# Kernel tuning notes

Hardware: AMD Instinct MI355X
Metric: run time of the kernel (lower is better)

The kernel has to match this reference:

```python
import jax, jax.numpy as jnp
import numpy as np

B, S, H, D = 8, 1024, 16, 64
W = H * D  # hidden width = 1024


def setup_inputs() -> dict:
    key = jax.random.key(0)
    ks = jax.random.split(key, 5)
    std = 0.02
    return {
        "from_tensor": jax.random.normal(ks[0], (B, S, W), dtype=jnp.float32),
        "to_tensor": jax.random.normal(ks[1], (B, S, W), dtype=jnp.float32),
        "Wq": jax.random.normal(ks[2], (W, W), dtype=jnp.float32) * std,
        "bq": jnp.zeros((W,), dtype=jnp.float32),
        "Wk": jax.random.normal(ks[3], (W, W), dtype=jnp.float32) * std,
        "bk": jnp.zeros((W,), dtype=jnp.float32),
        "Wv": jax.random.normal(ks[4], (W, W), dtype=jnp.float32) * std,
        "bv": jnp.zeros((W,), dtype=jnp.float32),
    }


def reference(from_tensor, to_tensor, Wq, bq, Wk, bk, Wv, bv):
    # Q/K/V projections (no activations: query_act=key_act=value_act=None)
    q = from_tensor @ Wq + bq  # [B, S, W]
    k = to_tensor @ Wk + bk
    v = to_tensor @ Wv + bv
    # split heads -> [B, H, S, D]
    q = q.reshape(B, S, H, D).transpose(0, 2, 1, 3)
    k = k.reshape(B, S, H, D).transpose(0, 2, 1, 3)
    v = v.reshape(B, S, H, D).transpose(0, 2, 1, 3)
    scale = 1.0 / np.sqrt(float(D))
    scores = jnp.einsum("bhqd,bhkd->bhqk", q, k) * scale  # [B, H, S, S]
    # attention_mask=None, dropout_prob=0.0 -> no mask, no dropout
    probs = jax.nn.softmax(scores, axis=-1)
    ctx = jnp.einsum("bhqk,bhkd->bhqd", probs, v)  # [B, H, S, D]
    # merge heads -> [B, S, H*D] (do_return_2d_tensor=False)
    return ctx.transpose(0, 2, 1, 3).reshape(B, S, H * D)
```

## Files before the change

### kernel.cpp

```cpp
#include <hip/hip_runtime.h>
#include <hip/hip_bf16.h>
#include <math.h>


#define B_ 8
#define S_ 1024
#define H_ 16
#define D_ 64
#define W_ 1024

typedef __bf16 bf16x8 __attribute__((ext_vector_type(8)));
typedef float f32x4 __attribute__((ext_vector_type(4)));
typedef unsigned short ushort_t;

#define MFMA16(a, b, c) __builtin_amdgcn_mfma_f32_16x16x32_bf16((a), (b), (c), 0, 0, 0)

__device__ inline ushort_t f2bf(float f) {
    unsigned int u = __float_as_uint(f);
    u += 0x7fff + ((u >> 16) & 1);
    return (ushort_t)(u >> 16);
}

__device__ inline unsigned f2bf_rhu_u(float f) {
    return (__float_as_uint(f) + 0x8000u) >> 16;
}

__device__ inline void async16(const void* g, void* l) {
    __builtin_amdgcn_global_load_lds((const __attribute__((address_space(1))) void*)g,
                                     (__attribute__((address_space(3))) void*)l, 16, 0, 0);
}

__global__ __launch_bounds__(256) void cast2_bf16(const float* __restrict__ a,
                                                  const float* __restrict__ b,
                                                  ushort_t* __restrict__ da,
                                                  ushort_t* __restrict__ db, int n4) {
    int i = blockIdx.x * 256 + threadIdx.x;
    if (i >= n4) return;
    const float* src = blockIdx.y ? b : a;
    ushort_t* dst = blockIdx.y ? db : da;
    float4 v = ((const float4*)src)[i];
    ushort4 o;
    o.x = f2bf(v.x); o.y = f2bf(v.y); o.z = f2bf(v.z); o.w = f2bf(v.w);
    ((ushort4*)dst)[i] = o;
}

__global__ __launch_bounds__(256) void transpose_cast(const float* __restrict__ Wq,
                                                      const float* __restrict__ Wk,
                                                      const float* __restrict__ Wv,
                                                      ushort_t* __restrict__ Wt) {
    __shared__ float tile[32][33];
    int z = blockIdx.z;
    const float* src = (z == 0) ? Wq : (z == 1 ? Wk : Wv);
    ushort_t* dst = Wt + (size_t)z * W_ * W_;
    int tx = threadIdx.x, ty = threadIdx.y;
    int x = blockIdx.x * 32 + tx;
#pragma unroll
    for (int jj = 0; jj < 4; jj++) {
        int y = blockIdx.y * 32 + ty + jj * 8;
        tile[ty + jj * 8][tx] = src[(size_t)y * W_ + x];
    }
    __syncthreads();
    int x2 = blockIdx.y * 32 + tx;
#pragma unroll
    for (int jj = 0; jj < 4; jj++) {
        int y2 = blockIdx.x * 32 + ty + jj * 8;
        dst[(size_t)y2 * W_ + x2] = f2bf(tile[tx][ty + jj * 8]);
    }
}

__global__ __launch_bounds__(256) void qkv_gemm(const ushort_t* __restrict__ fromB,
                                                const ushort_t* __restrict__ toB,
                                                const ushort_t* __restrict__ Wt,
                                                const float* __restrict__ bq,
                                                const float* __restrict__ bk,
                                                const float* __restrict__ bv,
                                                ushort_t* __restrict__ Qd,
                                                ushort_t* __restrict__ Kd,
                                                ushort_t* __restrict__ Vt) {
    __shared__ __attribute__((aligned(16))) ushort_t As[128 * 32];
    __shared__ __attribute__((aligned(16))) ushort_t Bs[128 * 32];
    int z = blockIdx.y;
    const ushort_t* A = (z == 0) ? fromB : toB;
    const ushort_t* Bt = Wt + (size_t)z * (W_ * W_);
    const float* bias = (z == 0) ? bq : (z == 1 ? bk : bv);
    ushort_t* dst = (z == 0) ? Qd : (z == 1 ? Kd : Vt);

    int bx = blockIdx.x;
    int j64 = bx >> 3;
    int mTile = ((bx & 7) << 3) | (j64 >> 3);
    int nTile = j64 & 7;
    int mBase = mTile * 128, nBase = nTile * 128;

    int t = threadIdx.x;
    int lane = t & 63, w = t >> 6;
    int wm = w >> 1, wn = w & 1;
    int ln = lane & 15, qd = lane >> 4;
    int wb = t & ~63;

    f32x4 zero = {0.f, 0.f, 0.f, 0.f};
    f32x4 acc[4][4];
#pragma unroll
    for (int i = 0; i < 4; i++)
#pragma unroll
        for (int j = 0; j < 4; j++) acc[i][j] = zero;

    for (int kt = 0; kt < 32; ++kt) {
        int k0 = kt * 32;
#pragma unroll
        for (int c = 0; c < 2; ++c) {
            int idx16 = c * 256 + t;
            int row = idx16 >> 2, seg = idx16 & 3;
            async16(A + (size_t)(mBase + row) * W_ + k0 + seg * 8, As + (size_t)(c * 256 + wb) * 8);
            async16(Bt + (size_t)(nBase + row) * W_ + k0 + seg * 8, Bs + (size_t)(c * 256 + wb) * 8);
        }
        __syncthreads();
        bf16x8 af[4], bfr[4];
#pragma unroll
        for (int i = 0; i < 4; i++) af[i] = *(const bf16x8*)(As + (wm * 64 + i * 16 + ln) * 32 + qd * 8);
#pragma unroll
        for (int j = 0; j < 4; j++) bfr[j] = *(const bf16x8*)(Bs + (wn * 64 + j * 16 + ln) * 32 + qd * 8);
#pragma unroll
        for (int i = 0; i < 4; i++)
#pragma unroll
            for (int j = 0; j < 4; j++) acc[i][j] = MFMA16(af[i], bfr[j], acc[i][j]);
        __syncthreads();
    }

#pragma unroll
    for (int j = 0; j < 4; j++) {
        int n = nBase + wn * 64 + j * 16 + ln;
        float bb = bias[n];
        int h = n >> 6, d = n & 63;
#pragma unroll
        for (int i = 0; i < 4; i++) {
            int mrow = mBase + wm * 64 + i * 16 + qd * 4;
#pragma unroll
            for (int r = 0; r < 4; r++) {
                int m = mrow + r;
                int b = m >> 10, s = m & 1023;
                float v = acc[i][j][r] + bb;
                if (z == 0) v *= 0.18033688011111773f;
                size_t idx;
                if (z < 2) idx = ((size_t)(b * H_ + h) * S_ + s) * D_ + d;
                else {
                    int sp = (s & ~63) | (s & 0x23) | ((s & 0x0C) << 1) | ((s & 0x10) >> 2);
                    idx = ((size_t)(b * H_ + h) * D_ + d) * S_ + sp;
                }
                dst[idx] = f2bf(v);
            }
        }
    }
}

__global__ __launch_bounds__(256, 3) void attn(const ushort_t* __restrict__ Qd,
                                               const ushort_t* __restrict__ Kd,
                                               const ushort_t* __restrict__ Vt,
                                               float* __restrict__ out) {
    __shared__ __attribute__((aligned(16))) ushort_t Ks[2][4096];
    __shared__ __attribute__((aligned(16))) ushort_t Vs[2][4096];

    int bh = blockIdx.y;
    int t = threadIdx.x, w = t >> 6, lane = t & 63;
    int ln = lane & 15, qd = lane >> 4;
    int qbase = blockIdx.x * 128 + w * 32;
    const ushort_t* Qb = Qd + (size_t)bh * S_ * D_;
    const ushort_t* Kb = Kd + (size_t)bh * S_ * D_;
    const ushort_t* Vb = Vt + (size_t)bh * D_ * S_;

    bf16x8 qf[2][2];
#pragma unroll
    for (int i = 0; i < 2; i++) {
        const ushort_t* qp = Qb + (size_t)(qbase + i * 16 + ln) * D_ + qd * 8;
        qf[i][0] = *(const bf16x8*)qp;
        qf[i][1] = *(const bf16x8*)(qp + 32);
    }

    int l8 = lane >> 3, s8 = lane & 7;
    int stgOff = (s8 ^ l8) << 3;
    const ushort_t* kg = Kb + (size_t)(w * 16 + l8) * D_ + stgOff;
    const ushort_t* vg = Vb + (size_t)(w * 16 + l8) * S_ + stgOff;
    int kOff = ln * 64 + ((qd ^ (ln & 7)) << 3);

    float rs[2] = {0.f, 0.f};
    f32x4 zero = {0.f, 0.f, 0.f, 0.f};
    f32x4 accO[2][4];
#pragma unroll
    for (int i = 0; i < 2; i++)
#pragma unroll
        for (int jd = 0; jd < 4; jd++) accO[i][jd] = zero;

    async16(kg, &Ks[0][w * 1024]);
    async16(kg + 8 * D_, &Ks[0][w * 1024 + 512]);
    async16(vg, &Vs[0][w * 1024]);
    async16(vg + 8 * S_, &Vs[0][w * 1024 + 512]);

    for (int c = 0; c < 16; ++c) {
        int buf = c & 1;
        __builtin_amdgcn_s_waitcnt(0x0F70);
        __syncthreads();
        if (c + 1 < 16) {
            int kc = (c + 1) * 64;
            async16(kg + (size_t)kc * D_, &Ks[buf ^ 1][w * 1024]);
            async16(kg + (size_t)kc * D_ + 8 * D_, &Ks[buf ^ 1][w * 1024 + 512]);
            async16(vg + kc, &Vs[buf ^ 1][w * 1024]);
            async16(vg + kc + 8 * S_, &Vs[buf ^ 1][w * 1024 + 512]);
        }

        f32x4 sc[2][4];
#pragma unroll
        for (int i = 0; i < 2; i++)
#pragma unroll
            for (int j = 0; j < 4; j++) sc[i][j] = zero;
        __builtin_amdgcn_s_setprio(1);
#pragma unroll
        for (int j = 0; j < 4; j++) {
            bf16x8 k0 = *(const bf16x8*)&Ks[buf][j * 1024 + kOff];
            bf16x8 k1 = *(const bf16x8*)&Ks[buf][(j * 1024 + kOff) ^ 32];
#pragma unroll
            for (int i = 0; i < 2; i++) {
                sc[i][j] = MFMA16(k0, qf[i][0], sc[i][j]);
                sc[i][j] = MFMA16(k1, qf[i][1], sc[i][j]);
            }
        }
        __builtin_amdgcn_s_setprio(0);

        bf16x8 pfrag[2][2];
#pragma unroll
        for (int i = 0; i < 2; i++)
#pragma unroll
            for (int m = 0; m < 2; m++) {
                union { unsigned u[4]; bf16x8 v; } pk;
#pragma unroll
                for (int jh = 0; jh < 2; jh++) {
                    float p0 = exp2f(sc[i][2 * m + jh][0]);
                    float p1 = exp2f(sc[i][2 * m + jh][1]);
                    float p2 = exp2f(sc[i][2 * m + jh][2]);
                    float p3 = exp2f(sc[i][2 * m + jh][3]);
                    rs[i] += (p0 + p1) + (p2 + p3);
                    pk.u[jh * 2]     = f2bf_rhu_u(p0) | (f2bf_rhu_u(p1) << 16);
                    pk.u[jh * 2 + 1] = f2bf_rhu_u(p2) | (f2bf_rhu_u(p3) << 16);
                }
                pfrag[i][m] = pk.v;
            }

        __builtin_amdgcn_s_setprio(1);
#pragma unroll
        for (int dt = 0; dt < 4; dt++)
#pragma unroll
            for (int m = 0; m < 2; m++) {
                bf16x8 vf = *(const bf16x8*)&Vs[buf][(dt * 16 + ln) * 64 +
                                                    ((((m << 2) + qd) ^ (ln & 7)) << 3)];
                accO[0][dt] = MFMA16(vf, pfrag[0][m], accO[0][dt]);
                accO[1][dt] = MFMA16(vf, pfrag[1][m], accO[1][dt]);
            }
        __builtin_amdgcn_s_setprio(0);
    }

    float inv[2];
#pragma unroll
    for (int i = 0; i < 2; i++) {
        float s = rs[i];
        s += __shfl_xor(s, 16);
        s += __shfl_xor(s, 32);
        inv[i] = 1.f / s;
    }
    int b = bh >> 4, h = bh & 15;
#pragma unroll
    for (int i = 0; i < 2; i++) {
        int q = qbase + i * 16 + ln;
        float* op = out + ((size_t)(b * S_ + q) * H_ + h) * D_ + qd * 4;
#pragma unroll
        for (int dt = 0; dt < 4; dt++) {
            float4 o4;
            o4.x = accO[i][dt][0] * inv[i];
            o4.y = accO[i][dt][1] * inv[i];
            o4.z = accO[i][dt][2] * inv[i];
            o4.w = accO[i][dt][3] * inv[i];
            *(float4*)(op + dt * 16) = o4;
        }
    }
}

extern "C" void kernel_launch(void* const* d_in, const int* in_sizes, int n_in,
                              void* d_out, int out_size, void* d_ws, size_t ws_size,
                              hipStream_t stream) {
    const float* from = (const float*)d_in[0];
    const float* to_  = (const float*)d_in[1];
    const float* Wq = (const float*)d_in[2];
    const float* bq = (const float*)d_in[3];
    const float* Wk = (const float*)d_in[4];
    const float* bk = (const float*)d_in[5];
    const float* Wv = (const float*)d_in[6];
    const float* bv = (const float*)d_in[7];
    float* out = (float*)d_out;

    const size_t NTOK = (size_t)B_ * S_ * W_;
    ushort_t* ws = (ushort_t*)d_ws;
    ushort_t* fromB = ws;
    ushort_t* toB = fromB + NTOK;
    ushort_t* Wt = toB + NTOK;
    ushort_t* Qd = Wt + (size_t)3 * W_ * W_;
    ushort_t* Kd = Qd + NTOK;
    ushort_t* Vt = Kd + NTOK;

    int n4 = (int)(NTOK / 4);
    cast2_bf16<<<dim3(n4 / 256, 2), dim3(256), 0, stream>>>(from, to_, fromB, toB, n4);
    transpose_cast<<<dim3(32, 32, 3), dim3(32, 8), 0, stream>>>(Wq, Wk, Wv, Wt);
    qkv_gemm<<<dim3(512, 3), dim3(256), 0, stream>>>(fromB, toB, Wt, bq, bk, bv, Qd, Kd, Vt);
    attn<<<dim3(8, 128), dim3(256), 0, stream>>>(Qd, Kd, Vt, out);
}
```

Measured before the change: 270.3 us.

## Merge prep kernels, remap attention grid, raise attention occupancy bound

```diff
diff --git a/kernel.cpp b/kernel.cpp
--- a/kernel.cpp
+++ b/kernel.cpp
@@ -30,40 +30,47 @@
                                      (__attribute__((address_space(3))) void*)l, 16, 0, 0);
 }
 
-__global__ __launch_bounds__(256) void cast2_bf16(const float* __restrict__ a,
-                                                  const float* __restrict__ b,
-                                                  ushort_t* __restrict__ da,
-                                                  ushort_t* __restrict__ db, int n4) {
-    int i = blockIdx.x * 256 + threadIdx.x;
-    if (i >= n4) return;
-    const float* src = blockIdx.y ? b : a;
-    ushort_t* dst = blockIdx.y ? db : da;
-    float4 v = ((const float4*)src)[i];
-    ushort4 o;
-    o.x = f2bf(v.x); o.y = f2bf(v.y); o.z = f2bf(v.z); o.w = f2bf(v.w);
-    ((ushort4*)dst)[i] = o;
-}
-
-__global__ __launch_bounds__(256) void transpose_cast(const float* __restrict__ Wq,
-                                                      const float* __restrict__ Wk,
-                                                      const float* __restrict__ Wv,
-                                                      ushort_t* __restrict__ Wt) {
+__global__ __launch_bounds__(256) void prep(const float* __restrict__ from,
+                                            const float* __restrict__ to_,
+                                            const float* __restrict__ Wq,
+                                            const float* __restrict__ Wk,
+                                            const float* __restrict__ Wv,
+                                            ushort_t* __restrict__ fromB,
+                                            ushort_t* __restrict__ toB,
+                                            ushort_t* __restrict__ Wt, int n4) {
+    int z = blockIdx.y;
+    int t = threadIdx.x;
+    if (z < 2) {
+        int i = blockIdx.x * 256 + t;
+        if (i >= n4) return;
+        const float* src = z ? to_ : from;
+        ushort_t* dst = z ? toB : fromB;
+        float4 v = ((const float4*)src)[i];
+        ushort4 o;
+        o.x = f2bf(v.x); o.y = f2bf(v.y); o.z = f2bf(v.z); o.w = f2bf(v.w);
+        ((ushort4*)dst)[i] = o;
+        return;
+    }
+    int bx = blockIdx.x;
+    if (bx >= 3072) return;
     __shared__ float tile[32][33];
-    int z = blockIdx.z;
-    const float* src = (z == 0) ? Wq : (z == 1 ? Wk : Wv);
-    ushort_t* dst = Wt + (size_t)z * W_ * W_;
-    int tx = threadIdx.x, ty = threadIdx.y;
-    int x = blockIdx.x * 32 + tx;
+    int zz = bx >> 10;
+    int tl = bx & 1023;
+    int bxx = tl & 31, byy = tl >> 5;
+    const float* src = (zz == 0) ? Wq : (zz == 1 ? Wk : Wv);
+    ushort_t* dst = Wt + (size_t)zz * W_ * W_;
+    int tx = t & 31, ty = t >> 5;
+    int x = bxx * 32 + tx;
 #pragma unroll
     for (int jj = 0; jj < 4; jj++) {
-        int y = blockIdx.y * 32 + ty + jj * 8;
+        int y = byy * 32 + ty + jj * 8;
         tile[ty + jj * 8][tx] = src[(size_t)y * W_ + x];
     }
     __syncthreads();
-    int x2 = blockIdx.y * 32 + tx;
+    int x2 = byy * 32 + tx;
 #pragma unroll
     for (int jj = 0; jj < 4; jj++) {
-        int y2 = blockIdx.x * 32 + ty + jj * 8;
+        int y2 = bxx * 32 + ty + jj * 8;
         dst[(size_t)y2 * W_ + x2] = f2bf(tile[tx][ty + jj * 8]);
     }
 }
@@ -152,17 +159,19 @@
     }
 }
 
-__global__ __launch_bounds__(256, 3) void attn(const ushort_t* __restrict__ Qd,
+__global__ __launch_bounds__(256, 4) void attn(const ushort_t* __restrict__ Qd,
                                                const ushort_t* __restrict__ Kd,
                                                const ushort_t* __restrict__ Vt,
                                                float* __restrict__ out) {
     __shared__ __attribute__((aligned(16))) ushort_t Ks[2][4096];
     __shared__ __attribute__((aligned(16))) ushort_t Vs[2][4096];
 
-    int bh = blockIdx.y;
+    int L = blockIdx.x;
+    int bh = ((L & 7) << 4) | ((L >> 3) & 15);
+    int qx = L >> 7;
     int t = threadIdx.x, w = t >> 6, lane = t & 63;
     int ln = lane & 15, qd = lane >> 4;
-    int qbase = blockIdx.x * 128 + w * 32;
+    int qbase = qx * 128 + w * 32;
     const ushort_t* Qb = Qd + (size_t)bh * S_ * D_;
     const ushort_t* Kb = Kd + (size_t)bh * S_ * D_;
     const ushort_t* Vb = Vt + (size_t)bh * D_ * S_;
@@ -304,8 +313,7 @@
     ushort_t* Vt = Kd + NTOK;
 
     int n4 = (int)(NTOK / 4);
-    cast2_bf16<<<dim3(n4 / 256, 2), dim3(256), 0, stream>>>(from, to_, fromB, toB, n4);
-    transpose_cast<<<dim3(32, 32, 3), dim3(32, 8), 0, stream>>>(Wq, Wk, Wv, Wt);
+    prep<<<dim3(n4 / 256, 3), dim3(256), 0, stream>>>(from, to_, Wq, Wk, Wv, fromB, toB, Wt, n4);
     qkv_gemm<<<dim3(512, 3), dim3(256), 0, stream>>>(fromB, toB, Wt, bq, bk, bv, Qd, Kd, Vt);
-    attn<<<dim3(8, 128), dim3(256), 0, stream>>>(Qd, Kd, Vt, out);
-}
+    attn<<<dim3(1024), dim3(256), 0, stream>>>(Qd, Kd, Vt, out);
+}
```

New measurement: 262.0 us. 3.1% less time.
